# Kernel tuning notes

Measured on AMD Instinct MI355X. Metric: run time of the kernel, lower is better.

The kernel has to match this reference:

```python
import jax, jax.numpy as jnp
import numpy as np
from jax import lax

# Model hyperparameters (match init_kwargs)
DIM = 512
N_HEADS = 8
HEAD_DIM = DIM // N_HEADS
N_LAYERS = 4
N_LEVELS = 3          # len(chunk_sizes); CMS forward = stack of MLPs per level
HIDDEN = 4 * DIM
VOCAB = 50257
MAX_SEQ = 2048
B, S = 1, 2048
LN_EPS = 1e-5


def layer_norm(x, w, b):
    m = x.mean(-1, keepdims=True)
    v = ((x - m) ** 2).mean(-1, keepdims=True)
    return (x - m) * lax.rsqrt(v + LN_EPS) * w + b


def linear_attention(x, wq, wk, wv, wo):
    """LinearAttentionWithMemory: fast-weight recurrence M += k v^T, ksum += k,
    y_t = (M_t q_t) / (ksum_t . q_t + 1e-6). x: (B,S,DIM). Weights stored (in,out)."""
    Bn, Sn, D = x.shape
    fmap = lambda z: jax.nn.elu(z) + 1.0  # elu(x)+1 feature map
    # (B,S,D) -> (S,B,H,d) for scan over time
    def proj(w):
        return fmap(x @ w).reshape(Bn, Sn, N_HEADS, HEAD_DIM).transpose(1, 0, 2, 3)
    q = proj(wq)
    k = proj(wk)
    v = fmap(x @ wv).reshape(Bn, Sn, N_HEADS, HEAD_DIM).transpose(1, 0, 2, 3)
    # NOTE: original applies feature_map only to Q and K; V is raw projection
    v = (x @ wv).reshape(Bn, Sn, N_HEADS, HEAD_DIM).transpose(1, 0, 2, 3)

    def step(carry, inp):
        M, ksum = carry            # M: (B,H,d,d), ksum: (B,H,d)
        q_t, k_t, v_t = inp        # each (B,H,d)
        M = M + k_t[..., :, None] * v_t[..., None, :]
        ksum = ksum + k_t
        num = jnp.einsum('bhde,bhd->bhe', M, q_t)
        den = jnp.einsum('bhd,bhd->bh', ksum, q_t)[..., None] + 1e-6
        return (M, ksum), num / den

    carry0 = (jnp.zeros((Bn, N_HEADS, HEAD_DIM, HEAD_DIM), x.dtype),
              jnp.zeros((Bn, N_HEADS, HEAD_DIM), x.dtype))
    _, ys = lax.scan(step, carry0, (q, k, v))          # ys: (S,B,H,d)
    out = ys.transpose(1, 0, 2, 3).reshape(Bn, Sn, D)
    return out @ wo


def cms(x, w1, b1, w2, b2):
    """Continuum Memory System forward: sequential chain of per-level MLPs
    (chunk sizes only control parameter-update frequency during training).
    w1: (N_LEVELS, DIM, HIDDEN), w2: (N_LEVELS, HIDDEN, DIM)."""
    h = x
    for lvl in range(N_LEVELS):
        h = jax.nn.gelu(h @ w1[lvl] + b1[lvl]) @ w2[lvl] + b2[lvl]
    return h


def setup_inputs() -> dict:
    key = jax.random.key(0)
    ks = jax.random.split(key, 16)
    std = 0.02
    inp = {
        'tok_emb': jax.random.normal(ks[0], (VOCAB, DIM), jnp.float32) * std,
        'pos_emb': jax.random.normal(ks[1], (MAX_SEQ, DIM), jnp.float32) * std,
        'ln1_w': jnp.ones((N_LAYERS, DIM), jnp.float32),
        'ln1_b': jnp.zeros((N_LAYERS, DIM), jnp.float32),
        'wq': jax.random.normal(ks[2], (N_LAYERS, DIM, DIM), jnp.float32) * std,
        'wk': jax.random.normal(ks[3], (N_LAYERS, DIM, DIM), jnp.float32) * std,
        'wv': jax.random.normal(ks[4], (N_LAYERS, DIM, DIM), jnp.float32) * std,
        'wo': jax.random.normal(ks[5], (N_LAYERS, DIM, DIM), jnp.float32) * std,
        'ln2_w': jnp.ones((N_LAYERS, DIM), jnp.float32),
        'ln2_b': jnp.zeros((N_LAYERS, DIM), jnp.float32),
        'cms_w1': jax.random.normal(ks[6], (N_LAYERS, N_LEVELS, DIM, HIDDEN), jnp.float32) * std,
        'cms_b1': jnp.zeros((N_LAYERS, N_LEVELS, HIDDEN), jnp.float32),
        'cms_w2': jax.random.normal(ks[7], (N_LAYERS, N_LEVELS, HIDDEN, DIM), jnp.float32) * std,
        'cms_b2': jnp.zeros((N_LAYERS, N_LEVELS, DIM), jnp.float32),
        'lnf_w': jnp.ones((DIM,), jnp.float32),
        'lnf_b': jnp.zeros((DIM,), jnp.float32),
        'input_ids': jax.random.randint(ks[8], (B, S), 0, VOCAB, jnp.int32),
    }
    return inp


def reference(tok_emb, pos_emb, ln1_w, ln1_b, wq, wk, wv, wo,
              ln2_w, ln2_b, cms_w1, cms_b1, cms_w2, cms_b2,
              lnf_w, lnf_b, input_ids):
    seq_len = input_ids.shape[1]
    x = tok_emb[input_ids] + pos_emb[:seq_len][None, :, :]
    for l in range(N_LAYERS):
        x = x + linear_attention(layer_norm(x, ln1_w[l], ln1_b[l]),
                                 wq[l], wk[l], wv[l], wo[l])
        x = x + cms(layer_norm(x, ln2_w[l], ln2_b[l]),
                    cms_w1[l], cms_b1[l], cms_w2[l], cms_b2[l])
    x = layer_norm(x, lnf_w, lnf_b)
    logits = x @ tok_emb.T  # tied head weights
    return logits
```

## Files before the change

### kernel.cpp

```cpp
#include <hip/hip_runtime.h>

#define SQL 2048
#define DIM 512
#define NHEADS 8
#define HD 64
#define NLAYERS 4
#define NLEVELS 3
#define HID 2048
#define VOC 50257
#define CHUNK 64
#define NCHUNK 32
#define SD (SQL * DIM)
#define DD (DIM * DIM)

typedef __attribute__((ext_vector_type(8))) short bf16x8;
typedef __attribute__((ext_vector_type(4))) float f32x4;

__device__ __forceinline__ float gelu_f(float x) {
    float x3 = x * x * x;
    return 0.5f * x * (1.f + tanhf(0.7978845608028654f * (x + 0.044715f * x3)));
}
__device__ __forceinline__ float fmap_f(float x) {
    return x > 0.f ? x + 1.f : expf(x);
}
__device__ __forceinline__ unsigned short f2bf(float x) {
    unsigned int u = __float_as_uint(x);
    u = (u + 0x7fffu + ((u >> 16) & 1u)) >> 16;
    return (unsigned short)u;
}
__device__ __forceinline__ float bf2f(unsigned short h) {
    return __uint_as_float(((unsigned int)h) << 16);
}

__global__ __launch_bounds__(256) void embed_k(
    const float* __restrict__ tok, const float* __restrict__ pos,
    const int* __restrict__ ids, float* __restrict__ x)
{
    int idx = blockIdx.x * 256 + threadIdx.x;
    int t = idx >> 9;
    int d = idx & 511;
    x[idx] = tok[(size_t)ids[t] * DIM + d] + pos[idx];
}

__global__ __launch_bounds__(256) void ln_k(
    const float* __restrict__ in, unsigned short* __restrict__ oh,
    unsigned short* __restrict__ ol,
    const float* __restrict__ w, const float* __restrict__ b)
{
    int t = blockIdx.x, tid = threadIdx.x;
    float v0 = in[t * DIM + tid];
    float v1 = in[t * DIM + 256 + tid];
    float s = v0 + v1, sq = v0 * v0 + v1 * v1;
    #pragma unroll
    for (int off = 32; off > 0; off >>= 1) {
        s  += __shfl_down(s, off);
        sq += __shfl_down(sq, off);
    }
    __shared__ float ss[4], sqs[4];
    int wave = tid >> 6, lane = tid & 63;
    if (lane == 0) { ss[wave] = s; sqs[wave] = sq; }
    __syncthreads();
    float S  = ss[0] + ss[1] + ss[2] + ss[3];
    float SQ = sqs[0] + sqs[1] + sqs[2] + sqs[3];
    float m   = S * (1.f / DIM);
    float var = SQ * (1.f / DIM) - m * m;
    float rs  = rsqrtf(var + 1e-5f);
    float y0 = (v0 - m) * rs * w[tid]       + b[tid];
    float y1 = (v1 - m) * rs * w[256 + tid] + b[256 + tid];
    unsigned short h0 = f2bf(y0), h1 = f2bf(y1);
    oh[t * DIM + tid]       = h0;
    ol[t * DIM + tid]       = f2bf(y0 - bf2f(h0));
    oh[t * DIM + 256 + tid] = h1;
    ol[t * DIM + 256 + tid] = f2bf(y1 - bf2f(h1));
}

__global__ __launch_bounds__(256) void conv_r_k(
    const float* __restrict__ in, unsigned short* __restrict__ oh,
    unsigned short* __restrict__ ol, long long n4)
{
    long long i = (long long)blockIdx.x * 256 + threadIdx.x;
    if (i >= n4) return;
    float4 v = ((const float4*)in)[i];
    unsigned short h0 = f2bf(v.x), h1 = f2bf(v.y), h2 = f2bf(v.z), h3 = f2bf(v.w);
    ushort4 hh; hh.x = h0; hh.y = h1; hh.z = h2; hh.w = h3;
    ushort4 ll;
    ll.x = f2bf(v.x - bf2f(h0));
    ll.y = f2bf(v.y - bf2f(h1));
    ll.z = f2bf(v.z - bf2f(h2));
    ll.w = f2bf(v.w - bf2f(h3));
    ((ushort4*)oh)[i] = hh;
    ((ushort4*)ol)[i] = ll;
}

__global__ __launch_bounds__(256) void conv_t_k(
    const float* __restrict__ in, unsigned short* __restrict__ oh,
    unsigned short* __restrict__ ol, int K, int N,
    size_t srcZ, size_t dstZ)
{
    in += (size_t)blockIdx.z * srcZ;
    oh += (size_t)blockIdx.z * dstZ;
    ol += (size_t)blockIdx.z * dstZ;
    __shared__ float T[32][33];
    const int n0 = blockIdx.x * 32, k0 = blockIdx.y * 32;
    const int tr = threadIdx.x >> 3, tc = threadIdx.x & 7;
    float4 v = *(const float4*)(in + (size_t)(k0 + tr) * N + n0 + tc * 4);
    T[tr][tc * 4 + 0] = v.x;
    T[tr][tc * 4 + 1] = v.y;
    T[tr][tc * 4 + 2] = v.z;
    T[tr][tc * 4 + 3] = v.w;
    __syncthreads();
    float o0 = T[tc * 4 + 0][tr];
    float o1 = T[tc * 4 + 1][tr];
    float o2 = T[tc * 4 + 2][tr];
    float o3 = T[tc * 4 + 3][tr];
    unsigned short h0 = f2bf(o0), h1 = f2bf(o1), h2 = f2bf(o2), h3 = f2bf(o3);
    ushort4 hh; hh.x = h0; hh.y = h1; hh.z = h2; hh.w = h3;
    ushort4 ll;
    ll.x = f2bf(o0 - bf2f(h0));
    ll.y = f2bf(o1 - bf2f(h1));
    ll.z = f2bf(o2 - bf2f(h2));
    ll.w = f2bf(o3 - bf2f(h3));
    size_t off = (size_t)(n0 + tr) * K + k0 + tc * 4;
    *(ushort4*)(oh + off) = hh;
    *(ushort4*)(ol + off) = ll;
}

template<int ACT, bool RES, bool PLANES, bool NG>
__global__ __launch_bounds__(256) void gemm_t(
    const unsigned short* __restrict__ Ah, const unsigned short* __restrict__ Al,
    const unsigned short* __restrict__ Bh, const unsigned short* __restrict__ Bl,
    const float* __restrict__ bias, const float* __restrict__ Rsrc,
    float* __restrict__ C, unsigned short* __restrict__ Oh,
    unsigned short* __restrict__ Ol,
    int M, int N, int K, int fthr)
{
    __shared__ unsigned short sAh[4096], sAl[4096], sBh[4096], sBl[4096];

    const int tid  = threadIdx.x;
    const int w    = tid >> 6, lane = tid & 63;
    const int r    = lane & 15, kq = lane >> 4;
    const int wr   = w >> 1, wc = w & 1;
    const int m0   = blockIdx.y * 128, n0 = blockIdx.x * 128;

    const int srow = tid >> 2;
    const int sch  = tid & 3;
    const int ar0 = m0 + srow, ar1 = ar0 + 64;
    int br0 = n0 + srow, br1 = br0 + 64;
    if (NG) { br0 = br0 < N ? br0 : N - 1; br1 = br1 < N ? br1 : N - 1; }
    const unsigned short* pAh0 = Ah + (size_t)ar0 * K + sch * 8;
    const unsigned short* pAh1 = Ah + (size_t)ar1 * K + sch * 8;
    const unsigned short* pAl0 = Al + (size_t)ar0 * K + sch * 8;
    const unsigned short* pAl1 = Al + (size_t)ar1 * K + sch * 8;
    const unsigned short* pBh0 = Bh + (size_t)br0 * K + sch * 8;
    const unsigned short* pBh1 = Bh + (size_t)br1 * K + sch * 8;
    const unsigned short* pBl0 = Bl + (size_t)br0 * K + sch * 8;
    const unsigned short* pBl1 = Bl + (size_t)br1 * K + sch * 8;

    bf16x8 rAh0 = *(const bf16x8*)pAh0, rAh1 = *(const bf16x8*)pAh1;
    bf16x8 rAl0 = *(const bf16x8*)pAl0, rAl1 = *(const bf16x8*)pAl1;
    bf16x8 rBh0 = *(const bf16x8*)pBh0, rBh1 = *(const bf16x8*)pBh1;
    bf16x8 rBl0 = *(const bf16x8*)pBl0, rBl1 = *(const bf16x8*)pBl1;

    f32x4 acc[4][4] = {};
    const int sw = tid * 8;

    for (int ks = 0; ks < K; ks += 32) {
        __syncthreads();
        *(bf16x8*)&sAh[sw] = rAh0;  *(bf16x8*)&sAh[sw + 2048] = rAh1;
        *(bf16x8*)&sAl[sw] = rAl0;  *(bf16x8*)&sAl[sw + 2048] = rAl1;
        *(bf16x8*)&sBh[sw] = rBh0;  *(bf16x8*)&sBh[sw + 2048] = rBh1;
        *(bf16x8*)&sBl[sw] = rBl0;  *(bf16x8*)&sBl[sw + 2048] = rBl1;
        __syncthreads();

        if (ks + 32 < K) {
            pAh0 += 32; pAh1 += 32; pAl0 += 32; pAl1 += 32;
            pBh0 += 32; pBh1 += 32; pBl0 += 32; pBl1 += 32;
            rAh0 = *(const bf16x8*)pAh0; rAh1 = *(const bf16x8*)pAh1;
            rAl0 = *(const bf16x8*)pAl0; rAl1 = *(const bf16x8*)pAl1;
            rBh0 = *(const bf16x8*)pBh0; rBh1 = *(const bf16x8*)pBh1;
            rBl0 = *(const bf16x8*)pBl0; rBl1 = *(const bf16x8*)pBl1;
        }

        bf16x8 a_h[4], a_l[4];
        #pragma unroll
        for (int mi = 0; mi < 4; ++mi) {
            const int off = (wr * 64 + mi * 16 + r) * 32 + kq * 8;
            a_h[mi] = *(const bf16x8*)&sAh[off];
            a_l[mi] = *(const bf16x8*)&sAl[off];
        }
        #pragma unroll
        for (int ni = 0; ni < 4; ++ni) {
            const int off = (wc * 64 + ni * 16 + r) * 32 + kq * 8;
            const bf16x8 b_h = *(const bf16x8*)&sBh[off];
            const bf16x8 b_l = *(const bf16x8*)&sBl[off];
            #pragma unroll
            for (int mi = 0; mi < 4; ++mi) {
                acc[mi][ni] = __builtin_amdgcn_mfma_f32_16x16x32_bf16(
                    a_h[mi], b_h, acc[mi][ni], 0, 0, 0);
                acc[mi][ni] = __builtin_amdgcn_mfma_f32_16x16x32_bf16(
                    a_h[mi], b_l, acc[mi][ni], 0, 0, 0);
                acc[mi][ni] = __builtin_amdgcn_mfma_f32_16x16x32_bf16(
                    a_l[mi], b_h, acc[mi][ni], 0, 0, 0);
            }
        }
    }

    #pragma unroll
    for (int mi = 0; mi < 4; ++mi)
        #pragma unroll
        for (int ni = 0; ni < 4; ++ni) {
            const int nn = n0 + wc * 64 + ni * 16 + r;
            if (NG && nn >= N) continue;
            #pragma unroll
            for (int g = 0; g < 4; ++g) {
                const int mm = m0 + wr * 64 + mi * 16 + kq * 4 + g;
                float v = acc[mi][ni][g];
                if (bias) v += bias[nn];
                if (ACT == 2) v = gelu_f(v);
                if (ACT == 3) v = (nn < fthr) ? fmap_f(v) : v;
                const size_t o = (size_t)mm * N + nn;
                if (PLANES) {
                    unsigned short h = f2bf(v);
                    Oh[o] = h;
                    Ol[o] = f2bf(v - bf2f(h));
                } else {
                    if (RES) v += Rsrc[o];
                    C[o] = v;
                }
            }
        }
}

template<int ACT, bool RES, bool PLANES>
__global__ __launch_bounds__(256) void gemm_ks(
    const unsigned short* __restrict__ Ah, const unsigned short* __restrict__ Al,
    const unsigned short* __restrict__ Bh, const unsigned short* __restrict__ Bl,
    const float* __restrict__ bias, const float* __restrict__ Rsrc,
    float* __restrict__ C, unsigned short* __restrict__ Oh,
    unsigned short* __restrict__ Ol,
    int M, int N, int K, int fthr)
{
    const int tid  = threadIdx.x;
    const int w    = tid >> 6;
    const int lane = tid & 63;
    const int r  = lane & 15;
    const int kq = lane >> 4;
    const int m0 = blockIdx.y * 64, n0 = blockIdx.x * 64;
    const int Kw = K >> 2;

    f32x4 acc[4][4] = {};

    size_t aoff[4], boff[4];
    #pragma unroll
    for (int i = 0; i < 4; ++i) {
        aoff[i] = (size_t)(m0 + i * 16 + r) * K + w * Kw + kq * 8;
        boff[i] = (size_t)(n0 + i * 16 + r) * K + w * Kw + kq * 8;
    }

    for (int k0 = 0; k0 < Kw; k0 += 32) {
        bf16x8 ah[4], al4[4], bh[4], bl4[4];
        #pragma unroll
        for (int i = 0; i < 4; ++i) {
            ah[i]  = *(const bf16x8*)(Ah + aoff[i] + k0);
            al4[i] = *(const bf16x8*)(Al + aoff[i] + k0);
            bh[i]  = *(const bf16x8*)(Bh + boff[i] + k0);
            bl4[i] = *(const bf16x8*)(Bl + boff[i] + k0);
        }
        #pragma unroll
        for (int mi = 0; mi < 4; ++mi)
            #pragma unroll
            for (int ni = 0; ni < 4; ++ni) {
                acc[mi][ni] = __builtin_amdgcn_mfma_f32_16x16x32_bf16(
                    ah[mi], bh[ni], acc[mi][ni], 0, 0, 0);
                acc[mi][ni] = __builtin_amdgcn_mfma_f32_16x16x32_bf16(
                    ah[mi], bl4[ni], acc[mi][ni], 0, 0, 0);
                acc[mi][ni] = __builtin_amdgcn_mfma_f32_16x16x32_bf16(
                    al4[mi], bh[ni], acc[mi][ni], 0, 0, 0);
            }
    }

    __shared__ f32x4 red[4][64][8];

    #pragma unroll
    for (int R = 0; R < 2; ++R) {
        if (R) __syncthreads();
        #pragma unroll
        for (int mh = 0; mh < 2; ++mh) {
            const int mi = R * 2 + mh;
            const int q2 = mh * 4 + kq;
            #pragma unroll
            for (int ni = 0; ni < 4; ++ni) {
                const int cc = ni * 16 + r;
                red[w][cc][q2 ^ (cc & 7)] = acc[mi][ni];
            }
        }
        __syncthreads();
        const int col = lane;
        #pragma unroll
        for (int g = 0; g < 2; ++g) {
            const int q2 = w * 2 + g;
            const int swz = q2 ^ (col & 7);
            f32x4 s = red[0][col][swz];
            s += red[1][col][swz];
            s += red[2][col][swz];
            s += red[3][col][swz];
            const int gn = n0 + col;
            float bv = bias ? bias[gn] : 0.f;
            #pragma unroll
            for (int e = 0; e < 4; ++e) {
                const int gm = m0 + R * 32 + q2 * 4 + e;
                float v = s[e] + bv;
                if (ACT == 2) v = gelu_f(v);
                if (ACT == 3) v = (gn < fthr) ? fmap_f(v) : v;
                const size_t o = (size_t)gm * N + gn;
                if (PLANES) {
                    unsigned short h = f2bf(v);
                    Oh[o] = h;
                    Ol[o] = f2bf(v - bf2f(h));
                } else {
                    if (RES) v += Rsrc[o];
                    C[o] = v;
                }
            }
        }
    }
}

__global__ __launch_bounds__(256) void attn_p1(
    const float* __restrict__ kbuf, const float* __restrict__ vbuf,
    float* __restrict__ Mc, float* __restrict__ ksum, int rs)
{
    const int h = blockIdx.x >> 5, c = blockIdx.x & 31;
    const int tid = threadIdx.x;
    const int tx = tid & 15, ty = tid >> 4;
    __shared__ float Ks[CHUNK][HD + 1];
    __shared__ float Vs[CHUNK][HD + 1];
    #pragma unroll
    for (int i = 0; i < 16; ++i) {
        int idx = tid + i * 256;
        int t = idx >> 6, d = idx & 63;
        size_t g = (size_t)(c * CHUNK + t) * rs + h * HD + d;
        Ks[t][d] = kbuf[g];
        Vs[t][d] = vbuf[g];
    }
    __syncthreads();

    float acc[4][4] = {};
    for (int t = 0; t < CHUNK; ++t) {
        float ka[4], vb[4];
        #pragma unroll
        for (int i = 0; i < 4; ++i) ka[i] = Ks[t][ty * 4 + i];
        #pragma unroll
        for (int j = 0; j < 4; ++j) vb[j] = Vs[t][tx * 4 + j];
        #pragma unroll
        for (int i = 0; i < 4; ++i)
            #pragma unroll
            for (int j = 0; j < 4; ++j)
                acc[i][j] += ka[i] * vb[j];
    }
    const size_t base = (size_t)(h * NCHUNK + c) * HD * HD;
    #pragma unroll
    for (int i = 0; i < 4; ++i)
        #pragma unroll
        for (int j = 0; j < 4; ++j)
            Mc[base + (size_t)(ty * 4 + i) * HD + tx * 4 + j] = acc[i][j];

    if (tid < HD) {
        float s = 0.f;
        for (int t = 0; t < CHUNK; ++t) s += Ks[t][tid];
        ksum[(size_t)(h * NCHUNK + c) * HD + tid] = s;
    }
}

__global__ __launch_bounds__(64) void attn_scan(
    float* __restrict__ Mc, float* __restrict__ ksum)
{
    const int b = blockIdx.x;
    const int h = b / 65, p = b % 65;
    const int tid = threadIdx.x;
    if (p < HD) {
        float run = 0.f;
        for (int c = 0; c < NCHUNK; ++c) {
            size_t idx = ((size_t)(h * NCHUNK + c) * HD + p) * HD + tid;
            float v = Mc[idx];
            Mc[idx] = run;
            run += v;
        }
    } else {
        float run = 0.f;
        for (int c = 0; c < NCHUNK; ++c) {
            size_t idx = (size_t)(h * NCHUNK + c) * HD + tid;
            float v = ksum[idx];
            ksum[idx] = run;
            run += v;
        }
    }
}

__global__ __launch_bounds__(256) void attn_p3(
    const float* __restrict__ qbuf, const float* __restrict__ kbuf,
    const float* __restrict__ vbuf, const float* __restrict__ Mc,
    const float* __restrict__ ksum,
    unsigned short* __restrict__ aoh, unsigned short* __restrict__ aol, int rs)
{
    const int h = blockIdx.x >> 5, c = blockIdx.x & 31;
    const int tid = threadIdx.x;
    const int tx = tid & 15, ty = tid >> 4;
    __shared__ float Qs[CHUNK][HD + 1];
    __shared__ float Ks[CHUNK][HD + 1];
    __shared__ float Vs[CHUNK][HD + 1];
    __shared__ float Ss[CHUNK][CHUNK + 1];
    __shared__ float Ms[HD][HD + 1];
    __shared__ float kp[HD], den[CHUNK];

    const size_t mbase = (size_t)(h * NCHUNK + c) * HD * HD;
    #pragma unroll
    for (int i = 0; i < 16; ++i) {
        int idx = tid + i * 256;
        int t = idx >> 6, d = idx & 63;
        size_t g = (size_t)(c * CHUNK + t) * rs + h * HD + d;
        Qs[t][d] = qbuf[g];
        Ks[t][d] = kbuf[g];
        Vs[t][d] = vbuf[g];
        Ms[t][d] = Mc[mbase + (size_t)t * HD + d];
    }
    if (tid < HD) kp[tid] = ksum[(size_t)(h * NCHUNK + c) * HD + tid];
    __syncthreads();

    {
        float acc[4][4] = {};
        for (int d = 0; d < HD; ++d) {
            float qa[4], kb[4];
            #pragma unroll
            for (int i = 0; i < 4; ++i) qa[i] = Qs[ty * 4 + i][d];
            #pragma unroll
            for (int j = 0; j < 4; ++j) kb[j] = Ks[tx * 4 + j][d];
            #pragma unroll
            for (int i = 0; i < 4; ++i)
                #pragma unroll
                for (int j = 0; j < 4; ++j)
                    acc[i][j] += qa[i] * kb[j];
        }
        #pragma unroll
        for (int i = 0; i < 4; ++i)
            #pragma unroll
            for (int j = 0; j < 4; ++j) {
                int t = ty * 4 + i, u = tx * 4 + j;
                Ss[t][u] = (u <= t) ? acc[i][j] : 0.f;
            }
    }
    __syncthreads();

    if (tid < CHUNK) {
        int t = tid;
        float s = 1e-6f;
        for (int d = 0; d < HD; ++d) s += Qs[t][d] * kp[d];
        for (int u = 0; u < CHUNK; ++u) s += Ss[t][u];
        den[t] = s;
    }
    __syncthreads();

    {
        float acc[4][4] = {};
        for (int d = 0; d < HD; ++d) {
            float qa[4], mb[4];
            #pragma unroll
            for (int i = 0; i < 4; ++i) qa[i] = Qs[ty * 4 + i][d];
            #pragma unroll
            for (int j = 0; j < 4; ++j) mb[j] = Ms[d][tx * 4 + j];
            #pragma unroll
            for (int i = 0; i < 4; ++i)
                #pragma unroll
                for (int j = 0; j < 4; ++j)
                    acc[i][j] += qa[i] * mb[j];
        }
        for (int u = 0; u < CHUNK; ++u) {
            float sa[4], vb[4];
            #pragma unroll
            for (int i = 0; i < 4; ++i) sa[i] = Ss[ty * 4 + i][u];
            #pragma unroll
            for (int j = 0; j < 4; ++j) vb[j] = Vs[u][tx * 4 + j];
            #pragma unroll
            for (int i = 0; i < 4; ++i)
                #pragma unroll
                for (int j = 0; j < 4; ++j)
                    acc[i][j] += sa[i] * vb[j];
        }
        #pragma unroll
        for (int i = 0; i < 4; ++i) {
            int t = ty * 4 + i;
            float inv = 1.f / den[t];
            #pragma unroll
            for (int j = 0; j < 4; ++j) {
                float vv = acc[i][j] * inv;
                unsigned short hh = f2bf(vv);
                size_t o = (size_t)(c * CHUNK + t) * DIM + h * HD + tx * 4 + j;
                aoh[o] = hh;
                aol[o] = f2bf(vv - bf2f(hh));
            }
        }
    }
}

extern "C" void kernel_launch(void* const* d_in, const int* in_sizes, int n_in,
                              void* d_out, int out_size, void* d_ws, size_t ws_size,
                              hipStream_t stream)
{
    const float* tok  = (const float*)d_in[0];
    const float* pos  = (const float*)d_in[1];
    const float* ln1w = (const float*)d_in[2];
    const float* ln1b = (const float*)d_in[3];
    const float* wq   = (const float*)d_in[4];
    const float* wk   = (const float*)d_in[5];
    const float* wv   = (const float*)d_in[6];
    const float* wo   = (const float*)d_in[7];
    const float* ln2w = (const float*)d_in[8];
    const float* ln2b = (const float*)d_in[9];
    const float* w1   = (const float*)d_in[10];
    const float* b1   = (const float*)d_in[11];
    const float* w2   = (const float*)d_in[12];
    const float* b2   = (const float*)d_in[13];
    const float* lnfw = (const float*)d_in[14];
    const float* lnfb = (const float*)d_in[15];
    const int*   ids  = (const int*)d_in[16];
    float* outp = (float*)d_out;

    typedef unsigned short us;
    char* p = (char*)d_ws;
    float* x   = (float*)p; p += (size_t)SD * 4;
    float* qkv = (float*)p; p += (size_t)SQL * 3 * DIM * 4;
    float* Mc  = (float*)p; p += (size_t)NHEADS * NCHUNK * HD * HD * 4;
    float* ksm = (float*)p; p += (size_t)NHEADS * NCHUNK * HD * 4;

    us* xnH = (us*)p; p += (size_t)SD * 2;
    us* xnL = (us*)p; p += (size_t)SD * 2;
    us* aoH = (us*)p; p += (size_t)SD * 2;
    us* aoL = (us*)p; p += (size_t)SD * 2;
    us* cinH = (us*)p; p += (size_t)SD * 2;
    us* cinL = (us*)p; p += (size_t)SD * 2;
    us* h1H = (us*)p; p += (size_t)SQL * HID * 2;
    us* h1L = (us*)p; p += (size_t)SQL * HID * 2;
    us* tokH = (us*)p; p += (size_t)VOC * DIM * 2;
    us* tokL = (us*)p; p += (size_t)VOC * DIM * 2;
    us* wqkvH = (us*)p; p += (size_t)NLAYERS * 3 * DD * 2;
    us* wqkvL = (us*)p; p += (size_t)NLAYERS * 3 * DD * 2;
    us* woH = (us*)p; p += (size_t)NLAYERS * DD * 2;
    us* woL = (us*)p; p += (size_t)NLAYERS * DD * 2;
    const size_t W1SZ = (size_t)NLAYERS * NLEVELS * DIM * HID;
    us* w1H = (us*)p; p += W1SZ * 2;
    us* w1L = (us*)p; p += W1SZ * 2;
    us* w2H = (us*)p; p += W1SZ * 2;
    us* w2L = (us*)p; p += W1SZ * 2;

    {
        long long n4 = (long long)VOC * DIM / 4;
        conv_r_k<<<(unsigned)((n4 + 255) / 256), 256, 0, stream>>>(tok, tokH, tokL, n4);
        dim3 gt(DIM / 32, DIM / 32, NLAYERS);
        conv_t_k<<<gt, 256, 0, stream>>>(wq, wqkvH,          wqkvL,          DIM, DIM, DD, (size_t)3 * DD);
        conv_t_k<<<gt, 256, 0, stream>>>(wk, wqkvH + DD,     wqkvL + DD,     DIM, DIM, DD, (size_t)3 * DD);
        conv_t_k<<<gt, 256, 0, stream>>>(wv, wqkvH + 2 * DD, wqkvL + 2 * DD, DIM, DIM, DD, (size_t)3 * DD);
        conv_t_k<<<gt, 256, 0, stream>>>(wo, woH, woL, DIM, DIM, DD, DD);
        dim3 g1(HID / 32, DIM / 32, NLAYERS * NLEVELS);
        conv_t_k<<<g1, 256, 0, stream>>>(w1, w1H, w1L, DIM, HID,
                                         (size_t)DIM * HID, (size_t)DIM * HID);
        dim3 g2(DIM / 32, HID / 32, NLAYERS * NLEVELS);
        conv_t_k<<<g2, 256, 0, stream>>>(w2, w2H, w2L, HID, DIM,
                                         (size_t)DIM * HID, (size_t)DIM * HID);
    }

    embed_k<<<SD / 256, 256, 0, stream>>>(tok, pos, ids, x);

    const dim3 gqkv(3 * DIM / 128, SQL / 128);
    const dim3 g512(DIM / 64, SQL / 64);
    const dim3 gw1(HID / 128, SQL / 128);
    const dim3 ghead((VOC + 127) / 128, SQL / 128);
    const int RS = 3 * DIM;

    for (int l = 0; l < NLAYERS; ++l) {
        ln_k<<<SQL, 256, 0, stream>>>(x, xnH, xnL, ln1w + l * DIM, ln1b + l * DIM);
        gemm_t<3, false, false, false><<<gqkv, 256, 0, stream>>>(
            xnH, xnL, wqkvH + (size_t)l * 3 * DD, wqkvL + (size_t)l * 3 * DD,
            nullptr, nullptr, qkv, nullptr, nullptr, SQL, 3 * DIM, DIM, 2 * DIM);
        attn_p1<<<NHEADS * NCHUNK, 256, 0, stream>>>(qkv + DIM, qkv + 2 * DIM, Mc, ksm, RS);
        attn_scan<<<NHEADS * 65, 64, 0, stream>>>(Mc, ksm);
        attn_p3<<<NHEADS * NCHUNK, 256, 0, stream>>>(
            qkv, qkv + DIM, qkv + 2 * DIM, Mc, ksm, aoH, aoL, RS);
        gemm_ks<0, true, false><<<g512, 256, 0, stream>>>(
            aoH, aoL, woH + (size_t)l * DD, woL + (size_t)l * DD,
            nullptr, x, x, nullptr, nullptr, SQL, DIM, DIM, 0);

        ln_k<<<SQL, 256, 0, stream>>>(x, xnH, xnL, ln2w + l * DIM, ln2b + l * DIM);
        const us* cH = xnH; const us* cL = xnL;
        for (int lvl = 0; lvl < NLEVELS; ++lvl) {
            const size_t off1 = (size_t)(l * NLEVELS + lvl) * DIM * HID;
            const float* b1p = b1 + (size_t)(l * NLEVELS + lvl) * HID;
            const float* b2p = b2 + (size_t)(l * NLEVELS + lvl) * DIM;
            gemm_t<2, false, true, false><<<gw1, 256, 0, stream>>>(
                cH, cL, w1H + off1, w1L + off1, b1p, nullptr,
                nullptr, h1H, h1L, SQL, HID, DIM, 0);
            if (lvl < NLEVELS - 1) {
                gemm_ks<0, false, true><<<g512, 256, 0, stream>>>(
                    h1H, h1L, w2H + off1, w2L + off1, b2p, nullptr,
                    nullptr, cinH, cinL, SQL, DIM, HID, 0);
                cH = cinH; cL = cinL;
            } else {
                gemm_ks<0, true, false><<<g512, 256, 0, stream>>>(
                    h1H, h1L, w2H + off1, w2L + off1, b2p, x,
                    x, nullptr, nullptr, SQL, DIM, HID, 0);
            }
        }
    }

    ln_k<<<SQL, 256, 0, stream>>>(x, xnH, xnL, lnfw, lnfb);
    gemm_t<0, false, false, true><<<ghead, 256, 0, stream>>>(
        xnH, xnL, tokH, tokL, nullptr, nullptr,
        outp, nullptr, nullptr, SQL, VOC, DIM, 0);
}
```

Before: 2.144 ms.

## Drop low bf16 plane for tied head weights and reorder head grid

The LM head GEMM now skips the B-low plane, doing two bf16 MFMAs per tile instead of three, and the vocab embedding is converted only to a high bf16 plane, which saves the conversion and the memory for the low plane. The head grid is swapped so consecutive blocks walk along M and share the same vocab tile, for better L2 reuse of B. The split-K GEMM is also software-pipelined with double-buffered register loads to overlap global loads with MFMAs. Dropping the a_h*b_l term lowers the precision of the logits slightly.

Result: faster. 2.093 ms (-2.4%).

```diff
diff --git a/kernel.cpp b/kernel.cpp
--- a/kernel.cpp
+++ b/kernel.cpp
@@ -74,22 +74,15 @@
     ol[t * DIM + 256 + tid] = f2bf(y1 - bf2f(h1));
 }
 
-__global__ __launch_bounds__(256) void conv_r_k(
-    const float* __restrict__ in, unsigned short* __restrict__ oh,
-    unsigned short* __restrict__ ol, long long n4)
+__global__ __launch_bounds__(256) void conv_rh_k(
+    const float* __restrict__ in, unsigned short* __restrict__ oh, long long n4)
 {
     long long i = (long long)blockIdx.x * 256 + threadIdx.x;
     if (i >= n4) return;
     float4 v = ((const float4*)in)[i];
-    unsigned short h0 = f2bf(v.x), h1 = f2bf(v.y), h2 = f2bf(v.z), h3 = f2bf(v.w);
-    ushort4 hh; hh.x = h0; hh.y = h1; hh.z = h2; hh.w = h3;
-    ushort4 ll;
-    ll.x = f2bf(v.x - bf2f(h0));
-    ll.y = f2bf(v.y - bf2f(h1));
-    ll.z = f2bf(v.z - bf2f(h2));
-    ll.w = f2bf(v.w - bf2f(h3));
+    ushort4 hh;
+    hh.x = f2bf(v.x); hh.y = f2bf(v.y); hh.z = f2bf(v.z); hh.w = f2bf(v.w);
     ((ushort4*)oh)[i] = hh;
-    ((ushort4*)ol)[i] = ll;
 }
 
 __global__ __launch_bounds__(256) void conv_t_k(
@@ -125,7 +118,7 @@
     *(ushort4*)(ol + off) = ll;
 }
 
-template<int ACT, bool RES, bool PLANES, bool NG>
+template<int ACT, bool RES, bool PLANES, bool NG, bool X3, bool MSWAP>
 __global__ __launch_bounds__(256) void gemm_t(
     const unsigned short* __restrict__ Ah, const unsigned short* __restrict__ Al,
     const unsigned short* __restrict__ Bh, const unsigned short* __restrict__ Bl,
@@ -134,13 +127,15 @@
     unsigned short* __restrict__ Ol,
     int M, int N, int K, int fthr)
 {
-    __shared__ unsigned short sAh[4096], sAl[4096], sBh[4096], sBl[4096];
+    __shared__ unsigned short sAh[4096], sAl[4096], sBh[4096];
+    __shared__ unsigned short sBl[X3 ? 4096 : 64];
 
     const int tid  = threadIdx.x;
     const int w    = tid >> 6, lane = tid & 63;
     const int r    = lane & 15, kq = lane >> 4;
     const int wr   = w >> 1, wc = w & 1;
-    const int m0   = blockIdx.y * 128, n0 = blockIdx.x * 128;
+    const int m0   = (MSWAP ? blockIdx.x : blockIdx.y) * 128;
+    const int n0   = (MSWAP ? blockIdx.y : blockIdx.x) * 128;
 
     const int srow = tid >> 2;
     const int sch  = tid & 3;
@@ -153,13 +148,14 @@
     const unsigned short* pAl1 = Al + (size_t)ar1 * K + sch * 8;
     const unsigned short* pBh0 = Bh + (size_t)br0 * K + sch * 8;
     const unsigned short* pBh1 = Bh + (size_t)br1 * K + sch * 8;
-    const unsigned short* pBl0 = Bl + (size_t)br0 * K + sch * 8;
-    const unsigned short* pBl1 = Bl + (size_t)br1 * K + sch * 8;
+    const unsigned short* pBl0 = X3 ? Bl + (size_t)br0 * K + sch * 8 : nullptr;
+    const unsigned short* pBl1 = X3 ? Bl + (size_t)br1 * K + sch * 8 : nullptr;
 
     bf16x8 rAh0 = *(const bf16x8*)pAh0, rAh1 = *(const bf16x8*)pAh1;
     bf16x8 rAl0 = *(const bf16x8*)pAl0, rAl1 = *(const bf16x8*)pAl1;
     bf16x8 rBh0 = *(const bf16x8*)pBh0, rBh1 = *(const bf16x8*)pBh1;
-    bf16x8 rBl0 = *(const bf16x8*)pBl0, rBl1 = *(const bf16x8*)pBl1;
+    bf16x8 rBl0, rBl1;
+    if constexpr (X3) { rBl0 = *(const bf16x8*)pBl0; rBl1 = *(const bf16x8*)pBl1; }
 
     f32x4 acc[4][4] = {};
     const int sw = tid * 8;
@@ -169,16 +165,21 @@
         *(bf16x8*)&sAh[sw] = rAh0;  *(bf16x8*)&sAh[sw + 2048] = rAh1;
         *(bf16x8*)&sAl[sw] = rAl0;  *(bf16x8*)&sAl[sw + 2048] = rAl1;
         *(bf16x8*)&sBh[sw] = rBh0;  *(bf16x8*)&sBh[sw + 2048] = rBh1;
-        *(bf16x8*)&sBl[sw] = rBl0;  *(bf16x8*)&sBl[sw + 2048] = rBl1;
+        if constexpr (X3) {
+            *(bf16x8*)&sBl[sw] = rBl0;  *(bf16x8*)&sBl[sw + 2048] = rBl1;
+        }
         __syncthreads();
 
         if (ks + 32 < K) {
             pAh0 += 32; pAh1 += 32; pAl0 += 32; pAl1 += 32;
-            pBh0 += 32; pBh1 += 32; pBl0 += 32; pBl1 += 32;
+            pBh0 += 32; pBh1 += 32;
             rAh0 = *(const bf16x8*)pAh0; rAh1 = *(const bf16x8*)pAh1;
             rAl0 = *(const bf16x8*)pAl0; rAl1 = *(const bf16x8*)pAl1;
             rBh0 = *(const bf16x8*)pBh0; rBh1 = *(const bf16x8*)pBh1;
-            rBl0 = *(const bf16x8*)pBl0; rBl1 = *(const bf16x8*)pBl1;
+            if constexpr (X3) {
+                pBl0 += 32; pBl1 += 32;
+                rBl0 = *(const bf16x8*)pBl0; rBl1 = *(const bf16x8*)pBl1;
+            }
         }
 
         bf16x8 a_h[4], a_l[4];
@@ -192,15 +193,19 @@
         for (int ni = 0; ni < 4; ++ni) {
             const int off = (wc * 64 + ni * 16 + r) * 32 + kq * 8;
             const bf16x8 b_h = *(const bf16x8*)&sBh[off];
-            const bf16x8 b_l = *(const bf16x8*)&sBl[off];
             #pragma unroll
             for (int mi = 0; mi < 4; ++mi) {
                 acc[mi][ni] = __builtin_amdgcn_mfma_f32_16x16x32_bf16(
                     a_h[mi], b_h, acc[mi][ni], 0, 0, 0);
                 acc[mi][ni] = __builtin_amdgcn_mfma_f32_16x16x32_bf16(
-                    a_h[mi], b_l, acc[mi][ni], 0, 0, 0);
-                acc[mi][ni] = __builtin_amdgcn_mfma_f32_16x16x32_bf16(
                     a_l[mi], b_h, acc[mi][ni], 0, 0, 0);
+            }
+            if constexpr (X3) {
+                const bf16x8 b_l = *(const bf16x8*)&sBl[off];
+                #pragma unroll
+                for (int mi = 0; mi < 4; ++mi)
+                    acc[mi][ni] = __builtin_amdgcn_mfma_f32_16x16x32_bf16(
+                        a_h[mi], b_l, acc[mi][ni], 0, 0, 0);
             }
         }
     }
@@ -257,27 +262,39 @@
         boff[i] = (size_t)(n0 + i * 16 + r) * K + w * Kw + kq * 8;
     }
 
-    for (int k0 = 0; k0 < Kw; k0 += 32) {
-        bf16x8 ah[4], al4[4], bh[4], bl4[4];
-        #pragma unroll
-        for (int i = 0; i < 4; ++i) {
-            ah[i]  = *(const bf16x8*)(Ah + aoff[i] + k0);
-            al4[i] = *(const bf16x8*)(Al + aoff[i] + k0);
-            bh[i]  = *(const bf16x8*)(Bh + boff[i] + k0);
-            bl4[i] = *(const bf16x8*)(Bl + boff[i] + k0);
-        }
-        #pragma unroll
-        for (int mi = 0; mi < 4; ++mi)
-            #pragma unroll
-            for (int ni = 0; ni < 4; ++ni) {
-                acc[mi][ni] = __builtin_amdgcn_mfma_f32_16x16x32_bf16(
-                    ah[mi], bh[ni], acc[mi][ni], 0, 0, 0);
-                acc[mi][ni] = __builtin_amdgcn_mfma_f32_16x16x32_bf16(
-                    ah[mi], bl4[ni], acc[mi][ni], 0, 0, 0);
-                acc[mi][ni] = __builtin_amdgcn_mfma_f32_16x16x32_bf16(
-                    al4[mi], bh[ni], acc[mi][ni], 0, 0, 0);
-            }
-    }
+#define KS_LD(ah_, al_, bh_, bl_, k0_) do {                        \
+    _Pragma("unroll")                                              \
+    for (int i = 0; i < 4; ++i) {                                  \
+        ah_[i] = *(const bf16x8*)(Ah + aoff[i] + (k0_));           \
+        al_[i] = *(const bf16x8*)(Al + aoff[i] + (k0_));           \
+        bh_[i] = *(const bf16x8*)(Bh + boff[i] + (k0_));           \
+        bl_[i] = *(const bf16x8*)(Bl + boff[i] + (k0_));           \
+    } } while (0)
+
+#define KS_MM(ah_, al_, bh_, bl_) do {                             \
+    _Pragma("unroll")                                              \
+    for (int mi = 0; mi < 4; ++mi)                                 \
+        _Pragma("unroll")                                          \
+        for (int ni = 0; ni < 4; ++ni) {                           \
+            acc[mi][ni] = __builtin_amdgcn_mfma_f32_16x16x32_bf16( \
+                ah_[mi], bh_[ni], acc[mi][ni], 0, 0, 0);           \
+            acc[mi][ni] = __builtin_amdgcn_mfma_f32_16x16x32_bf16( \
+                ah_[mi], bl_[ni], acc[mi][ni], 0, 0, 0);           \
+            acc[mi][ni] = __builtin_amdgcn_mfma_f32_16x16x32_bf16( \
+                al_[mi], bh_[ni], acc[mi][ni], 0, 0, 0);           \
+        } } while (0)
+
+    bf16x8 Pah[4], Pal[4], Pbh[4], Pbl[4];
+    bf16x8 Qah[4], Qal[4], Qbh[4], Qbl[4];
+    KS_LD(Pah, Pal, Pbh, Pbl, 0);
+    for (int k0 = 0; k0 < Kw; k0 += 64) {
+        if (k0 + 32 < Kw) KS_LD(Qah, Qal, Qbh, Qbl, k0 + 32);
+        KS_MM(Pah, Pal, Pbh, Pbl);
+        if (k0 + 64 < Kw) KS_LD(Pah, Pal, Pbh, Pbl, k0 + 64);
+        if (k0 + 32 < Kw) KS_MM(Qah, Qal, Qbh, Qbl);
+    }
+#undef KS_LD
+#undef KS_MM
 
     __shared__ f32x4 red[4][64][8];
 
@@ -541,7 +558,6 @@
     us* h1H = (us*)p; p += (size_t)SQL * HID * 2;
     us* h1L = (us*)p; p += (size_t)SQL * HID * 2;
     us* tokH = (us*)p; p += (size_t)VOC * DIM * 2;
-    us* tokL = (us*)p; p += (size_t)VOC * DIM * 2;
     us* wqkvH = (us*)p; p += (size_t)NLAYERS * 3 * DD * 2;
     us* wqkvL = (us*)p; p += (size_t)NLAYERS * 3 * DD * 2;
     us* woH = (us*)p; p += (size_t)NLAYERS * DD * 2;
@@ -554,7 +570,7 @@
 
     {
         long long n4 = (long long)VOC * DIM / 4;
-        conv_r_k<<<(unsigned)((n4 + 255) / 256), 256, 0, stream>>>(tok, tokH, tokL, n4);
+        conv_rh_k<<<(unsigned)((n4 + 255) / 256), 256, 0, stream>>>(tok, tokH, n4);
         dim3 gt(DIM / 32, DIM / 32, NLAYERS);
         conv_t_k<<<gt, 256, 0, stream>>>(wq, wqkvH,          wqkvL,          DIM, DIM, DD, (size_t)3 * DD);
         conv_t_k<<<gt, 256, 0, stream>>>(wk, wqkvH + DD,     wqkvL + DD,     DIM, DIM, DD, (size_t)3 * DD);
@@ -573,12 +589,12 @@
     const dim3 gqkv(3 * DIM / 128, SQL / 128);
     const dim3 g512(DIM / 64, SQL / 64);
     const dim3 gw1(HID / 128, SQL / 128);
-    const dim3 ghead((VOC + 127) / 128, SQL / 128);
+    const dim3 ghead(SQL / 128, (VOC + 127) / 128);
     const int RS = 3 * DIM;
 
     for (int l = 0; l < NLAYERS; ++l) {
         ln_k<<<SQL, 256, 0, stream>>>(x, xnH, xnL, ln1w + l * DIM, ln1b + l * DIM);
-        gemm_t<3, false, false, false><<<gqkv, 256, 0, stream>>>(
+        gemm_t<3, false, false, false, true, false><<<gqkv, 256, 0, stream>>>(
             xnH, xnL, wqkvH + (size_t)l * 3 * DD, wqkvL + (size_t)l * 3 * DD,
             nullptr, nullptr, qkv, nullptr, nullptr, SQL, 3 * DIM, DIM, 2 * DIM);
         attn_p1<<<NHEADS * NCHUNK, 256, 0, stream>>>(qkv + DIM, qkv + 2 * DIM, Mc, ksm, RS);
@@ -595,7 +611,7 @@
             const size_t off1 = (size_t)(l * NLEVELS + lvl) * DIM * HID;
             const float* b1p = b1 + (size_t)(l * NLEVELS + lvl) * HID;
             const float* b2p = b2 + (size_t)(l * NLEVELS + lvl) * DIM;
-            gemm_t<2, false, true, false><<<gw1, 256, 0, stream>>>(
+            gemm_t<2, false, true, false, true, false><<<gw1, 256, 0, stream>>>(
                 cH, cL, w1H + off1, w1L + off1, b1p, nullptr,
                 nullptr, h1H, h1L, SQL, HID, DIM, 0);
             if (lvl < NLEVELS - 1) {
@@ -612,7 +628,7 @@
     }
 
     ln_k<<<SQL, 256, 0, stream>>>(x, xnH, xnL, lnfw, lnfb);
-    gemm_t<0, false, false, true><<<ghead, 256, 0, stream>>>(
-        xnH, xnL, tokH, tokL, nullptr, nullptr,
+    gemm_t<0, false, false, true, false, true><<<ghead, 256, 0, stream>>>(
+        xnH, xnL, tokH, nullptr, nullptr, nullptr,
         outp, nullptr, nullptr, SQL, VOC, DIM, 0);
 }
```

## Drop low-bf16 plane for tied head weights; narrow N tiles; swap head grid order

Applied to the files above, without the earlier changes.

The LM-head GEMM now uses only the high bf16 plane of the token embedding, dropping the low-plane conversion, its storage, and one of three MFMAs per tile. That GEMM's grid is also transposed so consecutive blocks walk along M while sharing one vocab tile. The QKV and CMS-W1 GEMMs switch to 64-wide N tiles to launch more blocks. The prefix-scan kernel is unrolled to load all chunks before writing. Dropping the weight low plane reduces head accuracy toward plain bf16-times-split-activation precision.

Result: faster. 1.873 ms (-12.7%).

```diff
diff --git a/kernel.cpp b/kernel.cpp
--- a/kernel.cpp
+++ b/kernel.cpp
@@ -74,22 +74,15 @@
     ol[t * DIM + 256 + tid] = f2bf(y1 - bf2f(h1));
 }
 
-__global__ __launch_bounds__(256) void conv_r_k(
-    const float* __restrict__ in, unsigned short* __restrict__ oh,
-    unsigned short* __restrict__ ol, long long n4)
+__global__ __launch_bounds__(256) void conv_rh_k(
+    const float* __restrict__ in, unsigned short* __restrict__ oh, long long n4)
 {
     long long i = (long long)blockIdx.x * 256 + threadIdx.x;
     if (i >= n4) return;
     float4 v = ((const float4*)in)[i];
-    unsigned short h0 = f2bf(v.x), h1 = f2bf(v.y), h2 = f2bf(v.z), h3 = f2bf(v.w);
-    ushort4 hh; hh.x = h0; hh.y = h1; hh.z = h2; hh.w = h3;
-    ushort4 ll;
-    ll.x = f2bf(v.x - bf2f(h0));
-    ll.y = f2bf(v.y - bf2f(h1));
-    ll.z = f2bf(v.z - bf2f(h2));
-    ll.w = f2bf(v.w - bf2f(h3));
+    ushort4 hh;
+    hh.x = f2bf(v.x); hh.y = f2bf(v.y); hh.z = f2bf(v.z); hh.w = f2bf(v.w);
     ((ushort4*)oh)[i] = hh;
-    ((ushort4*)ol)[i] = ll;
 }
 
 __global__ __launch_bounds__(256) void conv_t_k(
@@ -125,7 +118,7 @@
     *(ushort4*)(ol + off) = ll;
 }
 
-template<int ACT, bool RES, bool PLANES, bool NG>
+template<int ACT, bool RES, bool PLANES, bool NG, bool X3, bool MSWAP, int BN>
 __global__ __launch_bounds__(256) void gemm_t(
     const unsigned short* __restrict__ Ah, const unsigned short* __restrict__ Al,
     const unsigned short* __restrict__ Bh, const unsigned short* __restrict__ Bl,
@@ -134,51 +127,75 @@
     unsigned short* __restrict__ Ol,
     int M, int N, int K, int fthr)
 {
-    __shared__ unsigned short sAh[4096], sAl[4096], sBh[4096], sBl[4096];
+    constexpr int NW = BN / 2;
+    constexpr int NF = NW / 16;
+    __shared__ unsigned short sAh[4096], sAl[4096];
+    __shared__ unsigned short sBh[BN * 32];
+    __shared__ unsigned short sBl[X3 ? BN * 32 : 64];
 
     const int tid  = threadIdx.x;
     const int w    = tid >> 6, lane = tid & 63;
     const int r    = lane & 15, kq = lane >> 4;
     const int wr   = w >> 1, wc = w & 1;
-    const int m0   = blockIdx.y * 128, n0 = blockIdx.x * 128;
+    const int m0   = (MSWAP ? blockIdx.x : blockIdx.y) * 128;
+    const int n0   = (MSWAP ? blockIdx.y : blockIdx.x) * BN;
 
     const int srow = tid >> 2;
     const int sch  = tid & 3;
     const int ar0 = m0 + srow, ar1 = ar0 + 64;
-    int br0 = n0 + srow, br1 = br0 + 64;
-    if (NG) { br0 = br0 < N ? br0 : N - 1; br1 = br1 < N ? br1 : N - 1; }
+    int br0 = n0 + srow;
+    if (NG) br0 = br0 < N ? br0 : N - 1;
     const unsigned short* pAh0 = Ah + (size_t)ar0 * K + sch * 8;
     const unsigned short* pAh1 = Ah + (size_t)ar1 * K + sch * 8;
     const unsigned short* pAl0 = Al + (size_t)ar0 * K + sch * 8;
     const unsigned short* pAl1 = Al + (size_t)ar1 * K + sch * 8;
     const unsigned short* pBh0 = Bh + (size_t)br0 * K + sch * 8;
-    const unsigned short* pBh1 = Bh + (size_t)br1 * K + sch * 8;
-    const unsigned short* pBl0 = Bl + (size_t)br0 * K + sch * 8;
-    const unsigned short* pBl1 = Bl + (size_t)br1 * K + sch * 8;
+    const unsigned short* pBl0 = X3 ? Bl + (size_t)br0 * K + sch * 8 : nullptr;
+    const unsigned short* pBh1 = nullptr;
+    const unsigned short* pBl1 = nullptr;
+    if constexpr (BN == 128) {
+        int br1 = n0 + 64 + srow;
+        if (NG) br1 = br1 < N ? br1 : N - 1;
+        pBh1 = Bh + (size_t)br1 * K + sch * 8;
+        if constexpr (X3) pBl1 = Bl + (size_t)br1 * K + sch * 8;
+    }
 
     bf16x8 rAh0 = *(const bf16x8*)pAh0, rAh1 = *(const bf16x8*)pAh1;
     bf16x8 rAl0 = *(const bf16x8*)pAl0, rAl1 = *(const bf16x8*)pAl1;
-    bf16x8 rBh0 = *(const bf16x8*)pBh0, rBh1 = *(const bf16x8*)pBh1;
-    bf16x8 rBl0 = *(const bf16x8*)pBl0, rBl1 = *(const bf16x8*)pBl1;
-
-    f32x4 acc[4][4] = {};
+    bf16x8 rBh0 = *(const bf16x8*)pBh0;
+    bf16x8 rBh1{}, rBl0{}, rBl1{};
+    if constexpr (X3) rBl0 = *(const bf16x8*)pBl0;
+    if constexpr (BN == 128) {
+        rBh1 = *(const bf16x8*)pBh1;
+        if constexpr (X3) rBl1 = *(const bf16x8*)pBl1;
+    }
+
+    f32x4 acc[4][NF] = {};
     const int sw = tid * 8;
 
     for (int ks = 0; ks < K; ks += 32) {
         __syncthreads();
         *(bf16x8*)&sAh[sw] = rAh0;  *(bf16x8*)&sAh[sw + 2048] = rAh1;
         *(bf16x8*)&sAl[sw] = rAl0;  *(bf16x8*)&sAl[sw + 2048] = rAl1;
-        *(bf16x8*)&sBh[sw] = rBh0;  *(bf16x8*)&sBh[sw + 2048] = rBh1;
-        *(bf16x8*)&sBl[sw] = rBl0;  *(bf16x8*)&sBl[sw + 2048] = rBl1;
+        *(bf16x8*)&sBh[sw] = rBh0;
+        if constexpr (BN == 128) *(bf16x8*)&sBh[sw + 2048] = rBh1;
+        if constexpr (X3) {
+            *(bf16x8*)&sBl[sw] = rBl0;
+            if constexpr (BN == 128) *(bf16x8*)&sBl[sw + 2048] = rBl1;
+        }
         __syncthreads();
 
         if (ks + 32 < K) {
             pAh0 += 32; pAh1 += 32; pAl0 += 32; pAl1 += 32;
-            pBh0 += 32; pBh1 += 32; pBl0 += 32; pBl1 += 32;
+            pBh0 += 32;
             rAh0 = *(const bf16x8*)pAh0; rAh1 = *(const bf16x8*)pAh1;
             rAl0 = *(const bf16x8*)pAl0; rAl1 = *(const bf16x8*)pAl1;
-            rBh0 = *(const bf16x8*)pBh0; rBh1 = *(const bf16x8*)pBh1;
-            rBl0 = *(const bf16x8*)pBl0; rBl1 = *(const bf16x8*)pBl1;
+            rBh0 = *(const bf16x8*)pBh0;
+            if constexpr (X3) { pBl0 += 32; rBl0 = *(const bf16x8*)pBl0; }
+            if constexpr (BN == 128) {
+                pBh1 += 32; rBh1 = *(const bf16x8*)pBh1;
+                if constexpr (X3) { pBl1 += 32; rBl1 = *(const bf16x8*)pBl1; }
+            }
         }
 
         bf16x8 a_h[4], a_l[4];
@@ -189,18 +206,22 @@
             a_l[mi] = *(const bf16x8*)&sAl[off];
         }
         #pragma unroll
-        for (int ni = 0; ni < 4; ++ni) {
-            const int off = (wc * 64 + ni * 16 + r) * 32 + kq * 8;
+        for (int ni = 0; ni < NF; ++ni) {
+            const int off = (wc * NW + ni * 16 + r) * 32 + kq * 8;
             const bf16x8 b_h = *(const bf16x8*)&sBh[off];
-            const bf16x8 b_l = *(const bf16x8*)&sBl[off];
             #pragma unroll
             for (int mi = 0; mi < 4; ++mi) {
                 acc[mi][ni] = __builtin_amdgcn_mfma_f32_16x16x32_bf16(
                     a_h[mi], b_h, acc[mi][ni], 0, 0, 0);
                 acc[mi][ni] = __builtin_amdgcn_mfma_f32_16x16x32_bf16(
-                    a_h[mi], b_l, acc[mi][ni], 0, 0, 0);
-                acc[mi][ni] = __builtin_amdgcn_mfma_f32_16x16x32_bf16(
                     a_l[mi], b_h, acc[mi][ni], 0, 0, 0);
+            }
+            if constexpr (X3) {
+                const bf16x8 b_l = *(const bf16x8*)&sBl[off];
+                #pragma unroll
+                for (int mi = 0; mi < 4; ++mi)
+                    acc[mi][ni] = __builtin_amdgcn_mfma_f32_16x16x32_bf16(
+                        a_h[mi], b_l, acc[mi][ni], 0, 0, 0);
             }
         }
     }
@@ -208,8 +229,8 @@
     #pragma unroll
     for (int mi = 0; mi < 4; ++mi)
         #pragma unroll
-        for (int ni = 0; ni < 4; ++ni) {
-            const int nn = n0 + wc * 64 + ni * 16 + r;
+        for (int ni = 0; ni < NF; ++ni) {
+            const int nn = n0 + wc * NW + ni * 16 + r;
             if (NG && nn >= N) continue;
             #pragma unroll
             for (int g = 0; g < 4; ++g) {
@@ -378,21 +399,28 @@
     const int b = blockIdx.x;
     const int h = b / 65, p = b % 65;
     const int tid = threadIdx.x;
+    float v[NCHUNK];
     if (p < HD) {
+        const size_t base = ((size_t)(h * NCHUNK) * HD + p) * HD + tid;
+        #pragma unroll
+        for (int c = 0; c < NCHUNK; ++c)
+            v[c] = Mc[base + (size_t)c * HD * HD];
         float run = 0.f;
+        #pragma unroll
         for (int c = 0; c < NCHUNK; ++c) {
-            size_t idx = ((size_t)(h * NCHUNK + c) * HD + p) * HD + tid;
-            float v = Mc[idx];
-            Mc[idx] = run;
-            run += v;
+            Mc[base + (size_t)c * HD * HD] = run;
+            run += v[c];
         }
     } else {
+        const size_t base = (size_t)(h * NCHUNK) * HD + tid;
+        #pragma unroll
+        for (int c = 0; c < NCHUNK; ++c)
+            v[c] = ksum[base + (size_t)c * HD];
         float run = 0.f;
+        #pragma unroll
         for (int c = 0; c < NCHUNK; ++c) {
-            size_t idx = (size_t)(h * NCHUNK + c) * HD + tid;
-            float v = ksum[idx];
-            ksum[idx] = run;
-            run += v;
+            ksum[base + (size_t)c * HD] = run;
+            run += v[c];
         }
     }
 }
@@ -541,7 +569,6 @@
     us* h1H = (us*)p; p += (size_t)SQL * HID * 2;
     us* h1L = (us*)p; p += (size_t)SQL * HID * 2;
     us* tokH = (us*)p; p += (size_t)VOC * DIM * 2;
-    us* tokL = (us*)p; p += (size_t)VOC * DIM * 2;
     us* wqkvH = (us*)p; p += (size_t)NLAYERS * 3 * DD * 2;
     us* wqkvL = (us*)p; p += (size_t)NLAYERS * 3 * DD * 2;
     us* woH = (us*)p; p += (size_t)NLAYERS * DD * 2;
@@ -554,7 +581,7 @@
 
     {
         long long n4 = (long long)VOC * DIM / 4;
-        conv_r_k<<<(unsigned)((n4 + 255) / 256), 256, 0, stream>>>(tok, tokH, tokL, n4);
+        conv_rh_k<<<(unsigned)((n4 + 255) / 256), 256, 0, stream>>>(tok, tokH, n4);
         dim3 gt(DIM / 32, DIM / 32, NLAYERS);
         conv_t_k<<<gt, 256, 0, stream>>>(wq, wqkvH,          wqkvL,          DIM, DIM, DD, (size_t)3 * DD);
         conv_t_k<<<gt, 256, 0, stream>>>(wk, wqkvH + DD,     wqkvL + DD,     DIM, DIM, DD, (size_t)3 * DD);
@@ -570,15 +597,15 @@
 
     embed_k<<<SD / 256, 256, 0, stream>>>(tok, pos, ids, x);
 
-    const dim3 gqkv(3 * DIM / 128, SQL / 128);
+    const dim3 gqkv(3 * DIM / 64, SQL / 128);
     const dim3 g512(DIM / 64, SQL / 64);
-    const dim3 gw1(HID / 128, SQL / 128);
-    const dim3 ghead((VOC + 127) / 128, SQL / 128);
+    const dim3 gw1(HID / 64, SQL / 128);
+    const dim3 ghead(SQL / 128, (VOC + 127) / 128);
     const int RS = 3 * DIM;
 
     for (int l = 0; l < NLAYERS; ++l) {
         ln_k<<<SQL, 256, 0, stream>>>(x, xnH, xnL, ln1w + l * DIM, ln1b + l * DIM);
-        gemm_t<3, false, false, false><<<gqkv, 256, 0, stream>>>(
+        gemm_t<3, false, false, false, true, false, 64><<<gqkv, 256, 0, stream>>>(
             xnH, xnL, wqkvH + (size_t)l * 3 * DD, wqkvL + (size_t)l * 3 * DD,
             nullptr, nullptr, qkv, nullptr, nullptr, SQL, 3 * DIM, DIM, 2 * DIM);
         attn_p1<<<NHEADS * NCHUNK, 256, 0, stream>>>(qkv + DIM, qkv + 2 * DIM, Mc, ksm, RS);
@@ -595,7 +622,7 @@
             const size_t off1 = (size_t)(l * NLEVELS + lvl) * DIM * HID;
             const float* b1p = b1 + (size_t)(l * NLEVELS + lvl) * HID;
             const float* b2p = b2 + (size_t)(l * NLEVELS + lvl) * DIM;
-            gemm_t<2, false, true, false><<<gw1, 256, 0, stream>>>(
+            gemm_t<2, false, true, false, true, false, 64><<<gw1, 256, 0, stream>>>(
                 cH, cL, w1H + off1, w1L + off1, b1p, nullptr,
                 nullptr, h1H, h1L, SQL, HID, DIM, 0);
             if (lvl < NLEVELS - 1) {
@@ -612,7 +639,7 @@
     }
 
     ln_k<<<SQL, 256, 0, stream>>>(x, xnH, xnL, lnfw, lnfb);
-    gemm_t<0, false, false, true><<<ghead, 256, 0, stream>>>(
-        xnH, xnL, tokH, tokL, nullptr, nullptr,
+    gemm_t<0, false, false, true, false, true, 128><<<ghead, 256, 0, stream>>>(
+        xnH, xnL, tokH, nullptr, nullptr, nullptr,
         outp, nullptr, nullptr, SQL, VOC, DIM, 0);
 }
```
